# Kernel optimization log

Measured on AMD Instinct MI355X. Metric: run time of the kernel, lower is better.

The kernel has to match this reference:

```python
import jax, jax.numpy as jnp
import numpy as np


def setup_inputs() -> dict:
    key = jax.random.key(0)
    k1, k2, k3 = jax.random.split(key, 3)
    B, T, D, H = 64, 1024, 256, 256
    x = jax.random.normal(k1, (B, T, D), dtype=jnp.float32)
    h0 = jnp.zeros((B, H), dtype=jnp.float32)
    # Keras 'random_normal' initializer uses stddev=0.05
    Wx = jax.random.normal(k2, (D, H), dtype=jnp.float32) * 0.05
    Wh = jax.random.normal(k3, (H, H), dtype=jnp.float32) * 0.05
    b = jnp.zeros((H,), dtype=jnp.float32)
    return {"x": x, "h0": h0, "Wx": Wx, "Wh": Wh, "b": b}


def reference(x, h0, Wx, Wh, b):
    # Vanilla RNN: h_t = tanh(x_t @ Wx + h_{t-1} @ Wh + b)
    # Hoist the input projection out of the recurrence (it has no sequential dep).
    xp = jnp.einsum('btd,dh->bth', x, Wx) + b  # [B,T,H]

    def step(h, xp_t):
        h_new = jnp.tanh(xp_t + h @ Wh)
        return h_new, h_new

    h_last, hs = jax.lax.scan(step, h0, jnp.swapaxes(xp, 0, 1))  # scan over T
    hs = jnp.swapaxes(hs, 0, 1)  # [B,T,H]
    return hs, h_last
```

## Files before the change

### kernel.cpp

```cpp
#include <hip/hip_runtime.h>

#define RNN_B 64
#define RNN_T 1024
#define RNN_D 256
#define RNN_H 256
#define NB 4
#define GEMM_ROWS 64

typedef __attribute__((ext_vector_type(8))) short bf16x8;
typedef __attribute__((ext_vector_type(4))) float f32x4;

__device__ __forceinline__ unsigned short f32_to_bf16_rne(float f) {
  unsigned u = __builtin_bit_cast(unsigned, f);
  u += 0x7fffu + ((u >> 16) & 1u);
  return (unsigned short)(u >> 16);
}

__device__ __forceinline__ float tanh_fast(float x) {
  const float e = x * 2.8853900817779268f;
  float t;
  asm("v_exp_f32 %0, %1" : "=v"(t) : "v"(e));
  const float r = __builtin_amdgcn_rcpf(t + 1.0f);
  return fmaf(-2.0f, r, 1.0f);
}

__device__ __forceinline__ int hidx(int batch, int col) {
  return ((batch & 7) * 512 + ((col * 2) ^ ((batch & 7) << 4))) >> 1;
}

__device__ __forceinline__ void wg_barrier_lds_only() {
  asm volatile("s_waitcnt lgkmcnt(0)" ::: "memory");
  __builtin_amdgcn_sched_barrier(0);
  __builtin_amdgcn_s_barrier();
  __builtin_amdgcn_sched_barrier(0);
}

__global__ __launch_bounds__(1024) void wx_prep_kernel(
    const float* __restrict__ Wx, unsigned short* __restrict__ Wxb) {
  const int g = blockIdx.x * 1024 + threadIdx.x;
  const int lq = g & 3;
  const int kc = (g >> 2) & 7;
  const int col = g >> 5;
  unsigned short v[8];
#pragma unroll
  for (int j = 0; j < 8; ++j) {
    const int k = kc * 32 + lq * 8 + j;
    v[j] = f32_to_bf16_rne(Wx[(size_t)k * RNN_H + col]);
  }
  *reinterpret_cast<uint4*>(&Wxb[(size_t)g * 8]) =
      *reinterpret_cast<const uint4*>(v);
}

__global__ __launch_bounds__(1024) void xp_gemm_mfma(
    const float* __restrict__ x, const unsigned short* __restrict__ Wxb,
    const float* __restrict__ bias, float* __restrict__ xp) {
  __shared__ unsigned short xs[GEMM_ROWS * 256];

  const int tid = threadIdx.x;
  const int wid = tid >> 6;
  const int lane = tid & 63;
  const int lrow = lane & 15;
  const int lq = lane >> 4;
  const size_t row0 = (size_t)blockIdx.x * GEMM_ROWS;

  bf16x8 wfrag[8];
  {
    const int col = wid * 16 + lrow;
#pragma unroll
    for (int kc = 0; kc < 8; ++kc)
      wfrag[kc] = *reinterpret_cast<const bf16x8*>(
          &Wxb[(size_t)((col * 8 + kc) * 4 + lq) * 8]);
  }
  const f32x4 bseed = *reinterpret_cast<const f32x4*>(&bias[wid * 16 + lq * 4]);

  {
    const int row = tid >> 4;
    const int c16 = (tid & 15) * 16;
    const float* src = x + (row0 + row) * RNN_D + c16;
    unsigned p[8];
#pragma unroll
    for (int q = 0; q < 4; ++q) {
      const f32x4 v = *reinterpret_cast<const f32x4*>(src + 4 * q);
      asm("v_cvt_pk_bf16_f32 %0, %1, %2" : "=v"(p[2 * q]) : "v"(v[0]), "v"(v[1]));
      asm("v_cvt_pk_bf16_f32 %0, %1, %2" : "=v"(p[2 * q + 1]) : "v"(v[2]), "v"(v[3]));
    }
    const int swz = (row & 7) << 4;
    const int b0 = row * 512 + ((c16 * 2) ^ swz);
    const int b1 = row * 512 + ((c16 * 2 + 16) ^ swz);
    *reinterpret_cast<uint4*>(&xs[b0 >> 1]) = *reinterpret_cast<uint4*>(&p[0]);
    *reinterpret_cast<uint4*>(&xs[b1 >> 1]) = *reinterpret_cast<uint4*>(&p[4]);
  }
  __syncthreads();

#pragma unroll
  for (int rg = 0; rg < GEMM_ROWS / 16; ++rg) {
    bf16x8 hf[8];
#pragma unroll
    for (int kc = 0; kc < 8; ++kc) {
      const int off =
          ((rg * 16 + lrow) * 512 + ((kc * 64 + lq * 16) ^ ((lrow & 7) << 4))) >> 1;
      hf[kc] = *reinterpret_cast<const bf16x8*>(&xs[off]);
    }
    f32x4 accE = bseed;
    f32x4 accO = {0.f, 0.f, 0.f, 0.f};
#pragma unroll
    for (int kc = 0; kc < 8; kc += 2) {
      accE = __builtin_amdgcn_mfma_f32_16x16x32_bf16(wfrag[kc], hf[kc], accE,
                                                     0, 0, 0);
      accO = __builtin_amdgcn_mfma_f32_16x16x32_bf16(wfrag[kc + 1], hf[kc + 1],
                                                     accO, 0, 0, 0);
    }
    const f32x4 r = accE + accO;
    float* dst = xp + (row0 + rg * 16 + lrow) * RNN_H + wid * 16 + lq * 4;
    *reinterpret_cast<f32x4*>(dst) = r;
  }
}

template <int SLOT>
__device__ __forceinline__ void rnn_step(
    unsigned short (&hb)[2][NB * 256], const bf16x8 (&wfrag)[8],
    f32x4 (&xq)[4], const float* xp_base, float* h_base, float* hl_st,
    bool last, bool act, int lrow, int lq, int wid) {
  constexpr int RD = SLOT & 1;
  const f32x4 xc = xq[SLOT];

  bf16x8 hf[8];
  if (act) {
#pragma unroll
    for (int kc = 0; kc < 8; ++kc) {
      const int off = (lrow * 512 + ((kc * 64 + lq * 16) ^ (lrow << 4))) >> 1;
      hf[kc] = *reinterpret_cast<const bf16x8*>(&hb[RD][off]);
    }
    xq[SLOT] = *reinterpret_cast<const f32x4*>(&xp_base[SLOT * RNN_H]);
  }

  f32x4 acc = xc;
  __builtin_amdgcn_s_setprio(1);
#pragma unroll
  for (int kc = 0; kc < 8; ++kc)
    acc = __builtin_amdgcn_mfma_f32_16x16x32_bf16(wfrag[kc], hf[kc], acc, 0, 0,
                                                  0);
  __builtin_amdgcn_s_setprio(0);

  f32x4 h;
#pragma unroll
  for (int r = 0; r < 4; ++r) h[r] = tanh_fast(acc[r]);
  if (act) {
    *reinterpret_cast<f32x4*>(&h_base[SLOT * RNN_H]) = h;
    if (last) *reinterpret_cast<f32x4*>(hl_st) = h;

    unsigned p0, p1;
    asm("v_cvt_pk_bf16_f32 %0, %1, %2" : "=v"(p0) : "v"(h[0]), "v"(h[1]));
    asm("v_cvt_pk_bf16_f32 %0, %1, %2" : "=v"(p1) : "v"(h[2]), "v"(h[3]));
    uint2 pk; pk.x = p0; pk.y = p1;
    const int byte = lrow * 512 + ((wid * 32 + lq * 8) ^ (lrow << 4));
    *reinterpret_cast<uint2*>(&hb[RD ^ 1][byte >> 1]) = pk;
  }

  wg_barrier_lds_only();
}

__global__ __launch_bounds__(1024, 4) void rnn_rec_mfma(
    const float* __restrict__ Wh, const float* __restrict__ h0, float* out,
    float* h_last) {
  __shared__ unsigned short hb[2][NB * 256];

  const int bg = blockIdx.x;
  const int tid = threadIdx.x;
  const int wid = tid >> 6;
  const int lane = tid & 63;
  const int lrow = lane & 15;
  const int lq = lane >> 4;
  const bool act = lrow < NB;

  bf16x8 wfrag[8];
  {
    const int col = wid * 16 + lrow;
#pragma unroll
    for (int kc = 0; kc < 8; ++kc) {
      bf16x8 v;
#pragma unroll
      for (int j = 0; j < 8; ++j) {
        const int k = kc * 32 + lq * 8 + j;
        v[j] = (short)f32_to_bf16_rne(Wh[(size_t)k * RNN_H + col]);
      }
      wfrag[kc] = v;
    }
  }

  {
    const int b = tid >> 8;
    const int c = tid & 255;
    hb[0][hidx(b, c)] =
        f32_to_bf16_rne(h0[(size_t)(bg * NB + b) * RNN_H + c]);
  }

  float* outb = out + (size_t)bg * NB * RNN_T * RNN_H;
  const int col0 = wid * 16 + lq * 4;
  float* hbase = outb + (size_t)(lrow & (NB - 1)) * RNN_T * RNN_H + col0;
  float* hl_st = h_last + (size_t)(bg * NB + (lrow & (NB - 1))) * RNN_H + col0;

  f32x4 xq[4];
  if (act) {
#pragma unroll
    for (int s = 0; s < 4; ++s)
      xq[s] = *reinterpret_cast<const f32x4*>(&hbase[s * RNN_H]);
  }
  const float* xp_base = hbase + 4 * RNN_H;
  float* h_base = hbase;

  wg_barrier_lds_only();

#pragma unroll 1
  for (int t = 0; t < RNN_T; t += 4) {
    const bool lastp = (t == RNN_T - 4);
    rnn_step<0>(hb, wfrag, xq, xp_base, h_base, hl_st, false, act, lrow, lq, wid);
    rnn_step<1>(hb, wfrag, xq, xp_base, h_base, hl_st, false, act, lrow, lq, wid);
    rnn_step<2>(hb, wfrag, xq, xp_base, h_base, hl_st, false, act, lrow, lq, wid);
    rnn_step<3>(hb, wfrag, xq, xp_base, h_base, hl_st, lastp, act, lrow, lq, wid);
    xp_base += 4 * RNN_H;
    h_base += 4 * RNN_H;
  }
}

extern "C" void kernel_launch(void* const* d_in, const int* in_sizes, int n_in,
                              void* d_out, int out_size, void* d_ws, size_t ws_size,
                              hipStream_t stream) {
  const float* x = (const float*)d_in[0];
  const float* h0 = (const float*)d_in[1];
  const float* Wx = (const float*)d_in[2];
  const float* Wh = (const float*)d_in[3];
  const float* bias = (const float*)d_in[4];
  float* out = (float*)d_out;
  float* h_last = out + (size_t)RNN_B * RNN_T * RNN_H;
  unsigned short* Wxb = (unsigned short*)d_ws;

  wx_prep_kernel<<<8, 1024, 0, stream>>>(Wx, Wxb);
  xp_gemm_mfma<<<RNN_B * RNN_T / GEMM_ROWS, 1024, 0, stream>>>(x, Wxb, bias,
                                                               out);
  rnn_rec_mfma<<<RNN_B / NB, 1024, 0, stream>>>(Wh, h0, out, h_last);
}
```

Before: 649.2 us.

## Pack 16 batches per recurrence block and give each wave two column tiles

The recurrence kernel now handles 16 batch rows per block instead of 4, so all 16 MFMA rows are active. It launches 4 blocks of 512 threads instead of 16 blocks of 1024. Each wave holds two Wh column fragments and issues two MFMA chains per step, so a step does more work with fewer waves per barrier. The cost is parallelism: only 4 workgroups run the serial recurrence, and each wave carries more register pressure and a longer per-step critical path.

```diff
diff --git a/kernel.cpp b/kernel.cpp
--- a/kernel.cpp
+++ b/kernel.cpp
@@ -4,7 +4,7 @@
 #define RNN_T 1024
 #define RNN_D 256
 #define RNN_H 256
-#define NB 4
+#define NB 16
 #define GEMM_ROWS 64
 
 typedef __attribute__((ext_vector_type(8))) short bf16x8;
@@ -25,7 +25,7 @@
 }
 
 __device__ __forceinline__ int hidx(int batch, int col) {
-  return ((batch & 7) * 512 + ((col * 2) ^ ((batch & 7) << 4))) >> 1;
+  return (batch * 512 + ((col * 2) ^ ((batch & 7) << 4))) >> 1;
 }
 
 __device__ __forceinline__ void wg_barrier_lds_only() {
@@ -118,49 +118,65 @@
 
 template <int SLOT>
 __device__ __forceinline__ void rnn_step(
-    unsigned short (&hb)[2][NB * 256], const bf16x8 (&wfrag)[8],
-    f32x4 (&xq)[4], const float* xp_base, float* h_base, float* hl_st,
-    bool last, bool act, int lrow, int lq, int wid) {
+    unsigned short (&hb)[2][NB * 256], const bf16x8 (&wfrag)[2][8],
+    f32x4 (&xq)[4][2], const float* xp_base, float* h_base, float* hl_st,
+    bool last, int lrow, int lq, int wid) {
   constexpr int RD = SLOT & 1;
-  const f32x4 xc = xq[SLOT];
+  const f32x4 xc0 = xq[SLOT][0];
+  const f32x4 xc1 = xq[SLOT][1];
 
   bf16x8 hf[8];
-  if (act) {
-#pragma unroll
-    for (int kc = 0; kc < 8; ++kc) {
-      const int off = (lrow * 512 + ((kc * 64 + lq * 16) ^ (lrow << 4))) >> 1;
-      hf[kc] = *reinterpret_cast<const bf16x8*>(&hb[RD][off]);
-    }
-    xq[SLOT] = *reinterpret_cast<const f32x4*>(&xp_base[SLOT * RNN_H]);
-  }
-
-  f32x4 acc = xc;
+#pragma unroll
+  for (int kc = 0; kc < 8; ++kc) {
+    const int off =
+        (lrow * 512 + ((kc * 64 + lq * 16) ^ ((lrow & 7) << 4))) >> 1;
+    hf[kc] = *reinterpret_cast<const bf16x8*>(&hb[RD][off]);
+  }
+  xq[SLOT][0] = *reinterpret_cast<const f32x4*>(&xp_base[SLOT * RNN_H]);
+  xq[SLOT][1] = *reinterpret_cast<const f32x4*>(&xp_base[SLOT * RNN_H + 16]);
+
+  f32x4 a0 = xc0, a1 = xc1;
   __builtin_amdgcn_s_setprio(1);
 #pragma unroll
-  for (int kc = 0; kc < 8; ++kc)
-    acc = __builtin_amdgcn_mfma_f32_16x16x32_bf16(wfrag[kc], hf[kc], acc, 0, 0,
-                                                  0);
+  for (int kc = 0; kc < 8; ++kc) {
+    a0 = __builtin_amdgcn_mfma_f32_16x16x32_bf16(wfrag[0][kc], hf[kc], a0, 0,
+                                                 0, 0);
+    a1 = __builtin_amdgcn_mfma_f32_16x16x32_bf16(wfrag[1][kc], hf[kc], a1, 0,
+                                                 0, 0);
+  }
   __builtin_amdgcn_s_setprio(0);
 
-  f32x4 h;
-#pragma unroll
-  for (int r = 0; r < 4; ++r) h[r] = tanh_fast(acc[r]);
-  if (act) {
-    *reinterpret_cast<f32x4*>(&h_base[SLOT * RNN_H]) = h;
-    if (last) *reinterpret_cast<f32x4*>(hl_st) = h;
-
-    unsigned p0, p1;
-    asm("v_cvt_pk_bf16_f32 %0, %1, %2" : "=v"(p0) : "v"(h[0]), "v"(h[1]));
-    asm("v_cvt_pk_bf16_f32 %0, %1, %2" : "=v"(p1) : "v"(h[2]), "v"(h[3]));
-    uint2 pk; pk.x = p0; pk.y = p1;
-    const int byte = lrow * 512 + ((wid * 32 + lq * 8) ^ (lrow << 4));
-    *reinterpret_cast<uint2*>(&hb[RD ^ 1][byte >> 1]) = pk;
+  f32x4 h0v, h1v;
+#pragma unroll
+  for (int r = 0; r < 4; ++r) {
+    h0v[r] = tanh_fast(a0[r]);
+    h1v[r] = tanh_fast(a1[r]);
+  }
+  *reinterpret_cast<f32x4*>(&h_base[SLOT * RNN_H]) = h0v;
+  *reinterpret_cast<f32x4*>(&h_base[SLOT * RNN_H + 16]) = h1v;
+  if (last) {
+    *reinterpret_cast<f32x4*>(hl_st) = h0v;
+    *reinterpret_cast<f32x4*>(hl_st + 16) = h1v;
+  }
+  {
+    unsigned p0, p1, p2, p3;
+    asm("v_cvt_pk_bf16_f32 %0, %1, %2" : "=v"(p0) : "v"(h0v[0]), "v"(h0v[1]));
+    asm("v_cvt_pk_bf16_f32 %0, %1, %2" : "=v"(p1) : "v"(h0v[2]), "v"(h0v[3]));
+    asm("v_cvt_pk_bf16_f32 %0, %1, %2" : "=v"(p2) : "v"(h1v[0]), "v"(h1v[1]));
+    asm("v_cvt_pk_bf16_f32 %0, %1, %2" : "=v"(p3) : "v"(h1v[2]), "v"(h1v[3]));
+    const int swz = (lrow & 7) << 4;
+    uint2 pk0; pk0.x = p0; pk0.y = p1;
+    uint2 pk1; pk1.x = p2; pk1.y = p3;
+    const int b0 = lrow * 512 + (((2 * wid) * 32 + lq * 8) ^ swz);
+    const int b1 = lrow * 512 + (((2 * wid + 1) * 32 + lq * 8) ^ swz);
+    *reinterpret_cast<uint2*>(&hb[RD ^ 1][b0 >> 1]) = pk0;
+    *reinterpret_cast<uint2*>(&hb[RD ^ 1][b1 >> 1]) = pk1;
   }
 
   wg_barrier_lds_only();
 }
 
-__global__ __launch_bounds__(1024, 4) void rnn_rec_mfma(
+__global__ __launch_bounds__(512, 2) void rnn_rec_mfma(
     const float* __restrict__ Wh, const float* __restrict__ h0, float* out,
     float* h_last) {
   __shared__ unsigned short hb[2][NB * 256];
@@ -171,11 +187,11 @@
   const int lane = tid & 63;
   const int lrow = lane & 15;
   const int lq = lane >> 4;
-  const bool act = lrow < NB;
-
-  bf16x8 wfrag[8];
-  {
-    const int col = wid * 16 + lrow;
+
+  bf16x8 wfrag[2][8];
+#pragma unroll
+  for (int i = 0; i < 2; ++i) {
+    const int col = (2 * wid + i) * 16 + lrow;
 #pragma unroll
     for (int kc = 0; kc < 8; ++kc) {
       bf16x8 v;
@@ -184,27 +200,30 @@
         const int k = kc * 32 + lq * 8 + j;
         v[j] = (short)f32_to_bf16_rne(Wh[(size_t)k * RNN_H + col]);
       }
-      wfrag[kc] = v;
-    }
-  }
-
-  {
-    const int b = tid >> 8;
-    const int c = tid & 255;
-    hb[0][hidx(b, c)] =
-        f32_to_bf16_rne(h0[(size_t)(bg * NB + b) * RNN_H + c]);
+      wfrag[i][kc] = v;
+    }
+  }
+
+  {
+    const int b = tid >> 5;
+    const int c0 = (tid & 31) * 8;
+#pragma unroll
+    for (int c = 0; c < 8; ++c) {
+      hb[0][hidx(b, c0 + c)] =
+          f32_to_bf16_rne(h0[(size_t)(bg * NB + b) * RNN_H + c0 + c]);
+    }
   }
 
   float* outb = out + (size_t)bg * NB * RNN_T * RNN_H;
-  const int col0 = wid * 16 + lq * 4;
-  float* hbase = outb + (size_t)(lrow & (NB - 1)) * RNN_T * RNN_H + col0;
-  float* hl_st = h_last + (size_t)(bg * NB + (lrow & (NB - 1))) * RNN_H + col0;
-
-  f32x4 xq[4];
-  if (act) {
-#pragma unroll
-    for (int s = 0; s < 4; ++s)
-      xq[s] = *reinterpret_cast<const f32x4*>(&hbase[s * RNN_H]);
+  const int col0 = (2 * wid) * 16 + lq * 4;
+  float* hbase = outb + (size_t)lrow * RNN_T * RNN_H + col0;
+  float* hl_st = h_last + (size_t)(bg * NB + lrow) * RNN_H + col0;
+
+  f32x4 xq[4][2];
+#pragma unroll
+  for (int s = 0; s < 4; ++s) {
+    xq[s][0] = *reinterpret_cast<const f32x4*>(&hbase[s * RNN_H]);
+    xq[s][1] = *reinterpret_cast<const f32x4*>(&hbase[s * RNN_H + 16]);
   }
   const float* xp_base = hbase + 4 * RNN_H;
   float* h_base = hbase;
@@ -214,10 +233,10 @@
 #pragma unroll 1
   for (int t = 0; t < RNN_T; t += 4) {
     const bool lastp = (t == RNN_T - 4);
-    rnn_step<0>(hb, wfrag, xq, xp_base, h_base, hl_st, false, act, lrow, lq, wid);
-    rnn_step<1>(hb, wfrag, xq, xp_base, h_base, hl_st, false, act, lrow, lq, wid);
-    rnn_step<2>(hb, wfrag, xq, xp_base, h_base, hl_st, false, act, lrow, lq, wid);
-    rnn_step<3>(hb, wfrag, xq, xp_base, h_base, hl_st, lastp, act, lrow, lq, wid);
+    rnn_step<0>(hb, wfrag, xq, xp_base, h_base, hl_st, false, lrow, lq, wid);
+    rnn_step<1>(hb, wfrag, xq, xp_base, h_base, hl_st, false, lrow, lq, wid);
+    rnn_step<2>(hb, wfrag, xq, xp_base, h_base, hl_st, false, lrow, lq, wid);
+    rnn_step<3>(hb, wfrag, xq, xp_base, h_base, hl_st, lastp, lrow, lq, wid);
     xp_base += 4 * RNN_H;
     h_base += 4 * RNN_H;
   }
@@ -238,5 +257,5 @@
   wx_prep_kernel<<<8, 1024, 0, stream>>>(Wx, Wxb);
   xp_gemm_mfma<<<RNN_B * RNN_T / GEMM_ROWS, 1024, 0, stream>>>(x, Wxb, bias,
                                                                out);
-  rnn_rec_mfma<<<RNN_B / NB, 1024, 0, stream>>>(Wh, h0, out, h_last);
-}
+  rnn_rec_mfma<<<RNN_B / NB, 512, 0, stream>>>(Wh, h0, out, h_last);
+}
```

After: 897.9 us. 38.3% more time.
